# Optimization experiments

Measured on AMD Instinct MI355X. Metric: run time of the kernel, lower is better.

Reference implementation:

```python
import math
import jax, jax.numpy as jnp
import numpy as np

D_MODEL = 4096
N_Q = 32
N_KV = 8
HEAD_DIM = D_MODEL // N_Q  # 128
N_REP = N_Q // N_KV        # 4
B, S = 2, 2048
NEG = -1e9


def setup_inputs() -> dict:
    key = jax.random.key(0)
    k = jax.random.split(key, 6)
    x = jax.random.normal(k[0], (B, S, D_MODEL), dtype=jnp.float32)
    # additive causal mask [1,1,S,S]
    causal = jnp.triu(jnp.full((S, S), NEG, dtype=jnp.float32), k=1)[None, None]
    qkv_out = HEAD_DIM * (N_Q + 2 * N_KV)  # 6144
    sc_in = 1.0 / math.sqrt(D_MODEL)
    Wqkv_w = jax.random.normal(k[1], (qkv_out, D_MODEL), dtype=jnp.float32) * sc_in
    Wqkv_b = jax.random.normal(k[2], (qkv_out,), dtype=jnp.float32) * 0.02
    out_w = jax.random.normal(k[3], (D_MODEL, D_MODEL), dtype=jnp.float32) * sc_in
    out_b = jax.random.normal(k[4], (D_MODEL,), dtype=jnp.float32) * 0.02
    return {"x": x, "attention_mask": causal, "Wqkv_w": Wqkv_w, "Wqkv_b": Wqkv_b,
            "out_w": out_w, "out_b": out_b}


def reference(x, attention_mask, Wqkv_w, Wqkv_b, out_w, out_b):
    bsz, seqlen, _ = x.shape
    qkv = x @ Wqkv_w.T + Wqkv_b                       # [B,S,(nq+2nkv)*hd]
    q_end = HEAD_DIM * N_Q
    k_end = q_end + HEAD_DIM * N_KV
    q = qkv[..., :q_end].reshape(bsz, seqlen, N_Q, HEAD_DIM)
    k = qkv[..., q_end:k_end].reshape(bsz, seqlen, N_KV, HEAD_DIM)
    v = qkv[..., k_end:].reshape(bsz, seqlen, N_KV, HEAD_DIM)
    # GQA: repeat each kv head n_rep times consecutively along head axis
    k = jnp.repeat(k, N_REP, axis=2)                  # [B,S,N_Q,hd]
    v = jnp.repeat(v, N_REP, axis=2)
    q = q.transpose(0, 2, 1, 3)                       # [B,H,S,hd]
    k = k.transpose(0, 2, 1, 3)
    v = v.transpose(0, 2, 1, 3)
    scores = jnp.einsum('bhqd,bhkd->bhqk', q, k) / math.sqrt(HEAD_DIM)
    scores = scores + attention_mask
    p = jax.nn.softmax(scores, axis=-1)
    out = jnp.einsum('bhqk,bhkd->bhqd', p, v)         # [B,H,S,hd]
    out = out.transpose(0, 2, 1, 3).reshape(bsz, seqlen, D_MODEL)
    return out @ out_w.T + out_b
```

## Files before the change

### kernel.cpp

```cpp
#include <hip/hip_runtime.h>

typedef unsigned short u16;
typedef unsigned int u32;
using f32x4  = __attribute__((ext_vector_type(4))) float;
using bf16x8 = __attribute__((ext_vector_type(8))) __bf16;
using u16x4  = __attribute__((ext_vector_type(4))) unsigned short;
using u16x8  = __attribute__((ext_vector_type(8))) unsigned short;
using u32x4  = __attribute__((ext_vector_type(4))) unsigned int;

#define MFMA16(a,b,c) __builtin_amdgcn_mfma_f32_16x16x32_bf16(a,b,c,0,0,0)

__device__ __forceinline__ u16 f2bf(float f) {
  unsigned u = __builtin_bit_cast(unsigned, f);
  u += 0x7FFFu + ((u >> 16) & 1u);
  return (u16)(u >> 16);
}
__device__ __forceinline__ u32 pk2(float a, float b) {
  return (u32)f2bf(a) | ((u32)f2bf(b) << 16);
}

__device__ __forceinline__ void gld_lds16(const void* g, void* l) {
  __builtin_amdgcn_global_load_lds(
      (const __attribute__((address_space(1))) unsigned*)g,
      (__attribute__((address_space(3))) unsigned*)l, 16, 0, 0);
}

__global__ __launch_bounds__(256) void cvt_f32_bf16(
    const float* __restrict__ in, u16* __restrict__ out, int n8) {
  int stride = gridDim.x * blockDim.x;
  for (int i = blockIdx.x * blockDim.x + threadIdx.x; i < n8; i += stride) {
    long e = (long)i * 8;
    f32x4 a = __builtin_nontemporal_load((const f32x4*)(in + e));
    f32x4 b = __builtin_nontemporal_load((const f32x4*)(in + e + 4));
    u16x8 r;
    r[0] = f2bf(a[0]); r[1] = f2bf(a[1]); r[2] = f2bf(a[2]); r[3] = f2bf(a[3]);
    r[4] = f2bf(b[0]); r[5] = f2bf(b[1]); r[6] = f2bf(b[2]); r[7] = f2bf(b[3]);
    *(u16x8*)(out + e) = r;
  }
}

template <int ROUTE>
__global__ __launch_bounds__(512, 2) void gemm256(
    const u16* __restrict__ A, const u16* __restrict__ Bw,
    const float* __restrict__ bias,
    u16* __restrict__ qkv, u16* __restrict__ vT, float* __restrict__ outF,
    int NBN) {
  extern __shared__ char sm[];
  constexpr int K = 4096, BK = 32, NT = K / BK;
  const int tid = threadIdx.x;

  const int bid = blockIdx.x;
  const int xcd = bid & 7;
  const int idx = bid >> 3;
  const int rm = idx & 7;
  const int rn = idx >> 3;
  const int m0 = ((xcd >> 2) * 8 + rm) * 256;
  const int n0 = ((xcd & 3) * (NBN >> 2) + rn) * 256;

  const int wid = tid >> 6, lane = tid & 63;
  const int wm = wid >> 2, wn = wid & 3;
  const int lr = lane & 15, lk = lane >> 4;

  auto stA = [&](int kt) {
    char* dst = sm + (kt & 3) * 32768;
    const int k0 = kt * BK;
#pragma unroll
    for (int i = 0; i < 2; ++i) {
      int p = (i * 512 + tid) * 16;
      int row = p >> 6, cb = p & 63;
      gld_lds16(A + (size_t)(m0 + row) * K + k0 +
                    ((cb ^ (((row >> 1) & 3) << 4)) >> 1),
                dst + p);
    }
  };
  auto stB = [&](int kt) {
    char* dst = sm + (kt & 3) * 32768 + 16384;
    const int k0 = kt * BK;
#pragma unroll
    for (int i = 0; i < 2; ++i) {
      int p = (i * 512 + tid) * 16;
      int row = p >> 6, cb = p & 63;
      gld_lds16(Bw + (size_t)(n0 + row) * K + k0 +
                    ((cb ^ (((row >> 1) & 3) << 4)) >> 1),
                dst + p);
    }
  };

  const int ck = (lk * 16) ^ (((lr >> 1) & 3) << 4);
  const int aRow = wm * 128 + lr;
  const int bRow = wn * 64 + lr;

  f32x4 acc[8][4] = {};
  bf16x8 bfr[4];

  stA(0); stB(0); stA(1); stB(1); stA(2); stB(2);
  asm volatile("s_waitcnt vmcnt(8)" ::: "memory");
  asm volatile("s_barrier" ::: "memory");

  for (int t = 0; t < NT; ++t) {
    const char* aB = sm + (t & 3) * 32768;
    const char* bB = aB + 16384;

    {
      bf16x8 afr[4];
#pragma unroll
      for (int n = 0; n < 4; ++n)
        bfr[n] = *(const bf16x8*)(bB + (bRow + n * 16) * 64 + ck);
#pragma unroll
      for (int mm = 0; mm < 4; ++mm)
        afr[mm] = *(const bf16x8*)(aB + (aRow + mm * 16) * 64 + ck);
      if (t + 3 < NT) stA(t + 3);
      asm volatile("s_barrier" ::: "memory");
      __builtin_amdgcn_s_setprio(1);
#pragma unroll
      for (int mm = 0; mm < 4; ++mm)
#pragma unroll
        for (int n = 0; n < 4; ++n)
          acc[mm][n] = MFMA16(afr[mm], bfr[n], acc[mm][n]);
      __builtin_amdgcn_s_setprio(0);
      asm volatile("s_barrier" ::: "memory");
    }
    {
      bf16x8 afr[4];
#pragma unroll
      for (int mm = 0; mm < 4; ++mm)
        afr[mm] = *(const bf16x8*)(aB + (aRow + (mm + 4) * 16) * 64 + ck);
      if (t + 3 < NT) stB(t + 3);
      asm volatile("s_barrier" ::: "memory");
      __builtin_amdgcn_s_setprio(1);
#pragma unroll
      for (int mm = 0; mm < 4; ++mm)
#pragma unroll
        for (int n = 0; n < 4; ++n)
          acc[mm + 4][n] = MFMA16(afr[mm], bfr[n], acc[mm + 4][n]);
      __builtin_amdgcn_s_setprio(0);
      if (t + 3 < NT)      asm volatile("s_waitcnt vmcnt(8)" ::: "memory");
      else if (t + 2 < NT) asm volatile("s_waitcnt vmcnt(4)" ::: "memory");
      else if (t + 1 < NT) asm volatile("s_waitcnt vmcnt(0)" ::: "memory");
      asm volatile("s_barrier" ::: "memory");
    }
  }

#pragma unroll
  for (int m = 0; m < 8; ++m) {
#pragma unroll
    for (int n = 0; n < 4; ++n) {
      const int col = n0 + wn * 64 + n * 16 + lr;
      const float bv = bias[col];
#pragma unroll
      for (int j = 0; j < 4; ++j) {
        const int row = m0 + wm * 128 + m * 16 + lk * 4 + j;
        const float v = acc[m][n][j] + bv;
        if (ROUTE == 0) {
          outF[(size_t)row * 4096 + col] = v;
        } else {
          if (col < 5120) {
            qkv[(size_t)row * 6144 + col] = f2bf(v);
          } else {
            int cv = col - 5120, hh = cv >> 7, d = cv & 127;
            int bb = row >> 11, s = row & 2047;
            vT[((size_t)((bb * 8 + hh) * 128 + d)) * 2048 + s] = f2bf(v);
          }
        }
      }
    }
  }
}

__global__ __launch_bounds__(256, 2) void attn_fwd(
    const u16* __restrict__ qkv, const u16* __restrict__ vT,
    u16* __restrict__ out) {
  __shared__ __align__(16) char smem[65536];

  const int tid = threadIdx.x;
  const int qt = blockIdx.x, h = blockIdx.y, b = blockIdx.z;
  const int hkv = h >> 2;
  const int q0 = qt * 128;
  const int wv = tid >> 6, lane = tid & 63;
  const int lr = lane & 15, lk = lane >> 4;

  auto stage = [&](int buf, int t) {
    const int kv0 = t * 64;
    char* kb_ = smem + buf * 32768;
    char* vb_ = kb_ + 16384;
#pragma unroll
    for (int i = 0; i < 4; ++i) {
      int c = i * 256 + tid, p = c * 16;
      int row = p >> 8, colb = (p & 255) ^ ((row & 7) << 4);
      gld_lds16(qkv + (size_t)(b * 2048 + kv0 + row) * 6144 + 4096 + hkv * 128 + (colb >> 1),
                kb_ + p);
    }
#pragma unroll
    for (int i = 0; i < 4; ++i) {
      int c = i * 256 + tid, p = c * 16;
      int row = p >> 7, colb = (p & 127) ^ ((row & 7) << 4);
      gld_lds16(vT + (size_t)((b * 8 + hkv) * 128 + row) * 2048 + kv0 + (colb >> 1),
                vb_ + p);
    }
  };

  bf16x8 qf[2][4];
#pragma unroll
  for (int qs = 0; qs < 2; ++qs) {
    const u16* qp = qkv + (size_t)(b * 2048 + q0 + wv * 32 + qs * 16 + lr) * 6144 +
                    h * 128 + lk * 8;
#pragma unroll
    for (int dc = 0; dc < 4; ++dc) qf[qs][dc] = *(const bf16x8*)(qp + dc * 32);
  }

  f32x4 o[2][8] = {};
  float mrun[2] = {-3.0e38f, -3.0e38f};
  float lsum[2] = {0.f, 0.f};
  const float sc = 0.08838834764831845f;

  const int nt = 2 * qt + 2;
  const int qbase_w = q0 + wv * 32;
  const int lkA = lr + 16 * (2 * (lk & 1) + (lk >> 1));
  const int lkB = lkA ^ 16;

  stage(0, 0);
  __syncthreads();
  for (int t = 0; t < nt; ++t) {
    const int buf = t & 1;
    if (t + 1 < nt) stage(buf ^ 1, t + 1);
    const int kv0 = t * 64;
    if (kv0 <= qbase_w + 31) {
      const char* kb_ = smem + buf * 32768;
      const char* vb_ = kb_ + 16384;

      f32x4 s[4][2];
#pragma unroll
      for (int cc = 0; cc < 4; ++cc) {
        const int krow = cc * 16 + lr;
        f32x4 a0 = {0.f, 0.f, 0.f, 0.f}, a1 = {0.f, 0.f, 0.f, 0.f};
#pragma unroll
        for (int dc = 0; dc < 4; ++dc) {
          bf16x8 kb = *(const bf16x8*)(kb_ + (krow << 8) +
                                       ((dc * 64 + lk * 16) ^ ((krow & 7) << 4)));
          a0 = MFMA16(kb, qf[0][dc], a0);
          a1 = MFMA16(kb, qf[1][dc], a1);
        }
        s[cc][0] = a0; s[cc][1] = a1;
      }

      const bool maskt = (kv0 + 63 > qbase_w);
#pragma unroll
      for (int cc = 0; cc < 4; ++cc)
#pragma unroll
        for (int qs = 0; qs < 2; ++qs)
#pragma unroll
          for (int j = 0; j < 4; ++j) {
            float v = s[cc][qs][j] * sc;
            if (maskt) {
              int kg = kv0 + cc * 16 + lk * 4 + j;
              int qg = qbase_w + qs * 16 + lr;
              if (kg > qg) v = -1.0e30f;
            }
            s[cc][qs][j] = v;
          }

      bf16x8 pfrag[2][2];
#pragma unroll
      for (int qs = 0; qs < 2; ++qs) {
        float mt = s[0][qs][0];
#pragma unroll
        for (int cc = 0; cc < 4; ++cc)
#pragma unroll
          for (int j = 0; j < 4; ++j) mt = fmaxf(mt, s[cc][qs][j]);
        mt = fmaxf(mt, __shfl_xor(mt, 16, 64));
        mt = fmaxf(mt, __shfl_xor(mt, 32, 64));
        const float mn = fmaxf(mrun[qs], mt);
        const float al = __expf(mrun[qs] - mn);
        mrun[qs] = mn;
        lsum[qs] *= al;
#pragma unroll
        for (int dc = 0; dc < 8; ++dc)
#pragma unroll
          for (int j = 0; j < 4; ++j) o[qs][dc][j] *= al;

        u32 pb[4][2];
        float ls = 0.f;
#pragma unroll
        for (int cc = 0; cc < 4; ++cc) {
          float p0 = __expf(s[cc][qs][0] - mn);
          float p1 = __expf(s[cc][qs][1] - mn);
          float p2 = __expf(s[cc][qs][2] - mn);
          float p3 = __expf(s[cc][qs][3] - mn);
          ls += (p0 + p1) + (p2 + p3);
          pb[cc][0] = pk2(p0, p1);
          pb[cc][1] = pk2(p2, p3);
        }
        lsum[qs] += ls;

#pragma unroll
        for (int ks = 0; ks < 2; ++ks) {
          const u32 e10 = (lk & 1) ? pb[ks * 2 + 1][0] : pb[ks * 2][0];
          const u32 e11 = (lk & 1) ? pb[ks * 2 + 1][1] : pb[ks * 2][1];
          const u32 e30 = (lk & 1) ? pb[ks * 2][0] : pb[ks * 2 + 1][0];
          const u32 e31 = (lk & 1) ? pb[ks * 2][1] : pb[ks * 2 + 1][1];
          const u32 r1 = __shfl((int)e10, lkA, 64);
          const u32 r2 = __shfl((int)e11, lkA, 64);
          const u32 r3 = __shfl((int)e30, lkB, 64);
          const u32 r4 = __shfl((int)e31, lkB, 64);
          u32x4 w;
          w[0] = (lk >> 1) ? r3 : r1;
          w[1] = (lk >> 1) ? r4 : r2;
          w[2] = (lk >> 1) ? r1 : r3;
          w[3] = (lk >> 1) ? r2 : r4;
          pfrag[qs][ks] = __builtin_bit_cast(bf16x8, w);
        }
      }

#pragma unroll
      for (int dc = 0; dc < 8; ++dc) {
        const int vrow = dc * 16 + lr;
#pragma unroll
        for (int ks = 0; ks < 2; ++ks) {
          bf16x8 vb = *(const bf16x8*)(vb_ + (vrow << 7) +
                                       ((ks * 64 + lk * 16) ^ ((vrow & 7) << 4)));
          o[0][dc] = MFMA16(vb, pfrag[0][ks], o[0][dc]);
          o[1][dc] = MFMA16(vb, pfrag[1][ks], o[1][dc]);
        }
      }
    }
    __syncthreads();
  }

  float rls[2];
#pragma unroll
  for (int qs = 0; qs < 2; ++qs) {
    float l = lsum[qs];
    l += __shfl_xor(l, 16, 64);
    l += __shfl_xor(l, 32, 64);
    rls[qs] = 1.0f / l;
  }
#pragma unroll
  for (int qs = 0; qs < 2; ++qs) {
    const int ql = wv * 32 + qs * 16 + lr;
#pragma unroll
    for (int dc = 0; dc < 8; ++dc) {
      u16x4 w;
#pragma unroll
      for (int j = 0; j < 4; ++j) w[j] = f2bf(o[qs][dc][j] * rls[qs]);
      *(u16x4*)(smem + ql * 256 + (((dc * 32 + lk * 8)) ^ ((ql & 7) << 4))) = w;
    }
  }
  __syncthreads();
#pragma unroll
  for (int i = 0; i < 8; ++i) {
    int c = i * 256 + tid;
    int row = c >> 4, ch = c & 15;
    u16x8 v = *(u16x8*)(smem + row * 256 + ((ch * 16) ^ ((row & 7) << 4)));
    *(u16x8*)(out + (size_t)(b * 2048 + q0 + row) * 4096 + h * 128 + ch * 8) = v;
  }
}

extern "C" void kernel_launch(void* const* d_in, const int* in_sizes, int n_in,
                              void* d_out, int out_size, void* d_ws, size_t ws_size,
                              hipStream_t stream) {
  const float* x  = (const float*)d_in[0];
  const float* w1 = (const float*)d_in[2];
  const float* b1 = (const float*)d_in[3];
  const float* w2 = (const float*)d_in[4];
  const float* b2 = (const float*)d_in[5];
  float* out = (float*)d_out;

  char* ws = (char*)d_ws;
  u16* xb   = (u16*)(ws);
  u16* w1b  = (u16*)(ws + 33554432ul);
  u16* w2b  = (u16*)(ws + 83886080ul);
  u16* qkv  = (u16*)(ws + 117440512ul);
  u16* vT   = (u16*)(ws + 167772160ul);
  u16* attnb = xb;

  (void)hipFuncSetAttribute(reinterpret_cast<const void*>(gemm256<1>),
                            hipFuncAttributeMaxDynamicSharedMemorySize, 131072);
  (void)hipFuncSetAttribute(reinterpret_cast<const void*>(gemm256<0>),
                            hipFuncAttributeMaxDynamicSharedMemorySize, 131072);

  cvt_f32_bf16<<<2048, 256, 0, stream>>>(x,  xb,  16777216 / 8);
  cvt_f32_bf16<<<2048, 256, 0, stream>>>(w1, w1b, 25165824 / 8);
  gemm256<1><<<384, 512, 131072, stream>>>(xb, w1b, b1, qkv, vT, nullptr, 24);
  cvt_f32_bf16<<<2048, 256, 0, stream>>>(w2, w2b, 16777216 / 8);
  attn_fwd<<<dim3(16, 32, 2), 256, 0, stream>>>(qkv, vT, attnb);
  gemm256<0><<<256, 512, 131072, stream>>>(attnb, w2b, b2, nullptr, nullptr, out, 16);
}
```

Before: 635.3 us.

## Replace 4-stage direct-to-LDS GEMM pipeline with register-staged double buffering

The GEMM main loop drops the four-buffer global_load_lds pipeline (128KB dynamic LDS) and uses a two-buffer static LDS scheme instead. Global tiles are prefetched two steps ahead into registers and written to LDS after each step's MFMAs, with one barrier per K step rather than several. This cuts LDS use to 64KB and the barrier count, but adds VGPR pressure and explicit ds_write traffic, and leaves a shallower prefetch depth to hide global latency.

New measurement: 630.3 us. No clear change (-0.8%).

```diff
diff --git a/kernel.cpp b/kernel.cpp
--- a/kernel.cpp
+++ b/kernel.cpp
@@ -45,8 +45,9 @@
     const float* __restrict__ bias,
     u16* __restrict__ qkv, u16* __restrict__ vT, float* __restrict__ outF,
     int NBN) {
-  extern __shared__ char sm[];
   constexpr int K = 4096, BK = 32, NT = K / BK;
+  __shared__ __align__(16) char lds[2][32768];
+
   const int tid = threadIdx.x;
 
   const int bid = blockIdx.x;
@@ -61,84 +62,74 @@
   const int wm = wid >> 2, wn = wid & 3;
   const int lr = lane & 15, lk = lane >> 4;
 
-  auto stA = [&](int kt) {
-    char* dst = sm + (kt & 3) * 32768;
-    const int k0 = kt * BK;
-#pragma unroll
-    for (int i = 0; i < 2; ++i) {
-      int p = (i * 512 + tid) * 16;
-      int row = p >> 6, cb = p & 63;
-      gld_lds16(A + (size_t)(m0 + row) * K + k0 +
-                    ((cb ^ (((row >> 1) & 3) << 4)) >> 1),
-                dst + p);
-    }
-  };
-  auto stB = [&](int kt) {
-    char* dst = sm + (kt & 3) * 32768 + 16384;
-    const int k0 = kt * BK;
-#pragma unroll
-    for (int i = 0; i < 2; ++i) {
-      int p = (i * 512 + tid) * 16;
-      int row = p >> 6, cb = p & 63;
-      gld_lds16(Bw + (size_t)(n0 + row) * K + k0 +
-                    ((cb ^ (((row >> 1) & 3) << 4)) >> 1),
-                dst + p);
-    }
-  };
+  const int r0 = tid >> 2, cc = tid & 3;
+  const u16* gA0 = A  + (size_t)(m0 + r0) * K + cc * 8;
+  const u16* gA1 = A  + (size_t)(m0 + 128 + r0) * K + cc * 8;
+  const u16* gB0 = Bw + (size_t)(n0 + r0) * K + cc * 8;
+  const u16* gB1 = Bw + (size_t)(n0 + 128 + r0) * K + cc * 8;
+  const int wsz = (((r0 >> 1) & 3) << 4);
+  const int wa0 = r0 * 64 + ((cc * 16) ^ wsz);
+  const int wa1 = wa0 + 128 * 64;
 
   const int ck = (lk * 16) ^ (((lr >> 1) & 3) << 4);
   const int aRow = wm * 128 + lr;
   const int bRow = wn * 64 + lr;
 
   f32x4 acc[8][4] = {};
-  bf16x8 bfr[4];
-
-  stA(0); stB(0); stA(1); stB(1); stA(2); stB(2);
-  asm volatile("s_waitcnt vmcnt(8)" ::: "memory");
-  asm volatile("s_barrier" ::: "memory");
-
-  for (int t = 0; t < NT; ++t) {
-    const char* aB = sm + (t & 3) * 32768;
+
+  auto step = [&](int t, u16x8& l0, u16x8& l1, u16x8& l2, u16x8& l3,
+                         u16x8& f0, u16x8& f1, u16x8& f2, u16x8& f3) {
+    if (t + 2 < NT) {
+      const int k0 = (t + 2) * BK;
+      f0 = *(const u16x8*)(gA0 + k0);
+      f1 = *(const u16x8*)(gA1 + k0);
+      f2 = *(const u16x8*)(gB0 + k0);
+      f3 = *(const u16x8*)(gB1 + k0);
+    }
+    const char* aB = lds[t & 1];
     const char* bB = aB + 16384;
-
-    {
-      bf16x8 afr[4];
+    bf16x8 afr[8], bfr[4];
+#pragma unroll
+    for (int n = 0; n < 4; ++n)
+      bfr[n] = *(const bf16x8*)(bB + (bRow + n * 16) * 64 + ck);
+#pragma unroll
+    for (int m = 0; m < 8; ++m)
+      afr[m] = *(const bf16x8*)(aB + (aRow + m * 16) * 64 + ck);
+    __builtin_amdgcn_s_setprio(1);
+#pragma unroll
+    for (int m = 0; m < 8; ++m)
 #pragma unroll
       for (int n = 0; n < 4; ++n)
-        bfr[n] = *(const bf16x8*)(bB + (bRow + n * 16) * 64 + ck);
-#pragma unroll
-      for (int mm = 0; mm < 4; ++mm)
-        afr[mm] = *(const bf16x8*)(aB + (aRow + mm * 16) * 64 + ck);
-      if (t + 3 < NT) stA(t + 3);
+        acc[m][n] = MFMA16(afr[m], bfr[n], acc[m][n]);
+    __builtin_amdgcn_s_setprio(0);
+    if (t + 1 < NT) {
+      char* dW = (char*)lds[(t + 1) & 1];
+      *(u16x8*)(dW + wa0) = l0;
+      *(u16x8*)(dW + wa1) = l1;
+      *(u16x8*)(dW + 16384 + wa0) = l2;
+      *(u16x8*)(dW + 16384 + wa1) = l3;
+      asm volatile("s_waitcnt lgkmcnt(0)" ::: "memory");
       asm volatile("s_barrier" ::: "memory");
-      __builtin_amdgcn_s_setprio(1);
-#pragma unroll
-      for (int mm = 0; mm < 4; ++mm)
-#pragma unroll
-        for (int n = 0; n < 4; ++n)
-          acc[mm][n] = MFMA16(afr[mm], bfr[n], acc[mm][n]);
-      __builtin_amdgcn_s_setprio(0);
-      asm volatile("s_barrier" ::: "memory");
-    }
-    {
-      bf16x8 afr[4];
-#pragma unroll
-      for (int mm = 0; mm < 4; ++mm)
-        afr[mm] = *(const bf16x8*)(aB + (aRow + (mm + 4) * 16) * 64 + ck);
-      if (t + 3 < NT) stB(t + 3);
-      asm volatile("s_barrier" ::: "memory");
-      __builtin_amdgcn_s_setprio(1);
-#pragma unroll
-      for (int mm = 0; mm < 4; ++mm)
-#pragma unroll
-        for (int n = 0; n < 4; ++n)
-          acc[mm + 4][n] = MFMA16(afr[mm], bfr[n], acc[mm + 4][n]);
-      __builtin_amdgcn_s_setprio(0);
-      if (t + 3 < NT)      asm volatile("s_waitcnt vmcnt(8)" ::: "memory");
-      else if (t + 2 < NT) asm volatile("s_waitcnt vmcnt(4)" ::: "memory");
-      else if (t + 1 < NT) asm volatile("s_waitcnt vmcnt(0)" ::: "memory");
-      asm volatile("s_barrier" ::: "memory");
-    }
+    }
+  };
+
+  u16x8 ra0, ra1, ra2, ra3, ea0, ea1, ea2, ea3;
+  ra0 = *(const u16x8*)(gA0); ra1 = *(const u16x8*)(gA1);
+  ra2 = *(const u16x8*)(gB0); ra3 = *(const u16x8*)(gB1);
+  ea0 = *(const u16x8*)(gA0 + BK); ea1 = *(const u16x8*)(gA1 + BK);
+  ea2 = *(const u16x8*)(gB0 + BK); ea3 = *(const u16x8*)(gB1 + BK);
+  {
+    char* dW = (char*)lds[0];
+    *(u16x8*)(dW + wa0) = ra0;
+    *(u16x8*)(dW + wa1) = ra1;
+    *(u16x8*)(dW + 16384 + wa0) = ra2;
+    *(u16x8*)(dW + 16384 + wa1) = ra3;
+    asm volatile("s_waitcnt lgkmcnt(0)" ::: "memory");
+    asm volatile("s_barrier" ::: "memory");
+  }
+  for (int t = 0; t < NT; t += 2) {
+    step(t,     ea0, ea1, ea2, ea3,  ra0, ra1, ra2, ra3);
+    step(t + 1, ra0, ra1, ra2, ra3,  ea0, ea1, ea2, ea3);
   }
 
 #pragma unroll
@@ -373,15 +364,10 @@
   u16* vT   = (u16*)(ws + 167772160ul);
   u16* attnb = xb;
 
-  (void)hipFuncSetAttribute(reinterpret_cast<const void*>(gemm256<1>),
-                            hipFuncAttributeMaxDynamicSharedMemorySize, 131072);
-  (void)hipFuncSetAttribute(reinterpret_cast<const void*>(gemm256<0>),
-                            hipFuncAttributeMaxDynamicSharedMemorySize, 131072);
-
   cvt_f32_bf16<<<2048, 256, 0, stream>>>(x,  xb,  16777216 / 8);
   cvt_f32_bf16<<<2048, 256, 0, stream>>>(w1, w1b, 25165824 / 8);
-  gemm256<1><<<384, 512, 131072, stream>>>(xb, w1b, b1, qkv, vT, nullptr, 24);
+  gemm256<1><<<384, 512, 0, stream>>>(xb, w1b, b1, qkv, vT, nullptr, 24);
   cvt_f32_bf16<<<2048, 256, 0, stream>>>(w2, w2b, 16777216 / 8);
   attn_fwd<<<dim3(16, 32, 2), 256, 0, stream>>>(qkv, vT, attnb);
-  gemm256<0><<<256, 512, 131072, stream>>>(attnb, w2b, b2, nullptr, nullptr, out, 16);
-}
+  gemm256<0><<<256, 512, 0, stream>>>(attnb, w2b, b2, nullptr, nullptr, out, 16);
+}
```
